# Optimization experiments

Measured on AMD Instinct MI355X. Metric: run time of the kernel, lower is better.

Reference implementation:

```python
import jax, jax.numpy as jnp
import numpy as np

N, E, W, H, NXF, NDF = 131072, 8, 128, 64, 10, 4
DX = 3 + 3 * 2 * NXF  # 63
DV = 3 + 3 * 2 * NDF  # 27
TEMP = 0.166667


def pe(x, degree):
    # positional encoding: [x, sin(2^i x), cos(2^i x)]
    y = jnp.concatenate([(2.0 ** i) * x for i in range(degree)], -1)
    return jnp.concatenate([x, jnp.sin(y), jnp.cos(y)], -1)


def setup_inputs() -> dict:
    key = jax.random.key(0)
    ks = jax.random.split(key, 8)
    s = 0.05
    return {
        'x': jax.random.normal(ks[0], (N, 6), jnp.float32),
        'W_enc': jax.random.normal(ks[1], (DX, W), jnp.float32) * s,
        'b_enc': jnp.zeros((W,), jnp.float32),
        'W_sh': jax.random.normal(ks[2], (E, W, W), jnp.float32) * s,
        'b_sh': jnp.zeros((E, W), jnp.float32),
        'w_sig': jax.random.normal(ks[3], (W,), jnp.float32) * s,
        'b_sig': jnp.zeros((1,), jnp.float32),
        'W_r1': jax.random.normal(ks[4], (E, W + DV, H), jnp.float32) * s,
        'b_r1': jnp.zeros((E, H), jnp.float32),
        'W_r2': jax.random.normal(ks[5], (E, H, 3), jnp.float32) * s,
        'b_r2': jnp.zeros((E, 3), jnp.float32),
    }


def reference(x, W_enc, b_enc, W_sh, b_sh, w_sig, b_sig, W_r1, b_r1, W_r2, b_r2):
    xyz = pe(x[:, :3], NXF)          # [N, 63]
    vd = pe(x[:, 3:6], NDF)          # [N, 27]
    y = jax.nn.relu(xyz @ W_enc + b_enc)  # encoding_xyz -> [N, W]
    # all shape experts at once: [N, E, W]
    shape_out = jax.nn.relu(jnp.einsum('nd,edh->neh', y, W_sh) + b_sh)
    # shared sigma head, softplus keeps sigma > 0: [N, E]
    sigmas = jax.nn.softplus(jnp.einsum('neh,h->ne', shape_out, w_sig) + b_sig)
    log_logits = jax.nn.log_softmax(jnp.log(sigmas + 1e-10) / TEMP, axis=-1)
    # gumbel-softmax (tau=1, torch default) with fixed noise key
    u = jax.random.uniform(jax.random.key(42), sigmas.shape, jnp.float32)
    g = -jnp.log(-jnp.log(u + 1e-20) + 1e-20)
    gates_soft = jax.nn.softmax(log_logits + g, axis=-1)
    index = jnp.argmax(gates_soft, axis=-1)  # [N]
    hard = jax.nn.one_hot(index, E, dtype=sigmas.dtype)
    # straight-through hard gates
    gates_hard = hard - jax.lax.stop_gradient(gates_soft) + gates_soft
    sigmas_pooled = jnp.take_along_axis(sigmas, index[:, None], axis=-1)  # [N, 1]
    # rgb experts: concat(shape_out_i, viewdir) -> MLP -> sigmoid rgb, gated sum
    vdb = jnp.broadcast_to(vd[:, None, :], (vd.shape[0], E, DV))
    inp = jnp.concatenate([shape_out, vdb], axis=-1)  # [N, E, W+27]
    h = jax.nn.relu(jnp.einsum('nec,ech->neh', inp, W_r1) + b_r1)
    rgb = jax.nn.sigmoid(jnp.einsum('neh,eho->neo', h, W_r2) + b_r2)  # [N, E, 3]
    rgbs = jnp.sum(rgb * gates_hard[:, :, None], axis=1)  # [N, 3]
    return jnp.concatenate([rgbs, sigmas_pooled], axis=-1)  # [N, 4]
```

## Files before the change

### kernel.cpp

```cpp
#include <hip/hip_runtime.h>
#include <hip/hip_bf16.h>


#define NPTS 131072
#define PT 64
#define NTH 256
#define NBLK (NPTS / PT)
#define INV2048 (1.0f / 2048.0f)

#define WS_ENC_H 0
#define WS_ENC_L 8192
#define WS_SH_H  16384
#define WS_SH_L  147456
#define WS_R1_H  278528

#define OFF_YH   0
#define OFF_B    17408
#define OFF_RED  38912
#define SMEM_SZ  40960

#define S_LIST(s) (*(int*)(smem + OFF_B + (s) * 336 + 320))
#define S_BID(p)  (*(int*)(smem + OFF_B + (p) * 336 + 324))
#define S_CNT(e)  (*(int*)(smem + OFF_B + (e) * 336 + 328))
#define S_OFF(e)  (*(int*)(smem + OFF_B + (e) * 336 + 332))

typedef __attribute__((ext_vector_type(8))) _Float16 f16x8;
typedef __attribute__((ext_vector_type(4))) _Float16 f16x4;
typedef __attribute__((ext_vector_type(4))) float f32x4;

#define MFMA(a, b, c) __builtin_amdgcn_mfma_f32_16x16x32_f16((a), (b), (c), 0, 0, 0)

__device__ __forceinline__ unsigned rotl32(unsigned x, int d) {
  return (x << d) | (x >> (32 - d));
}

__device__ __forceinline__ float gumbel_for(unsigned flat) {
  const unsigned k0 = 0u, k1 = 42u;
  const unsigned ks2 = k0 ^ k1 ^ 0x1BD11BDAu;
  unsigned x0 = 0u + k0;
  unsigned x1 = flat + k1;
#define TF_RND(r) { x0 += x1; x1 = rotl32(x1, r); x1 ^= x0; }
  TF_RND(13) TF_RND(15) TF_RND(26) TF_RND(6)
  x0 += k1;  x1 += ks2 + 1u;
  TF_RND(17) TF_RND(29) TF_RND(16) TF_RND(24)
  x0 += ks2; x1 += k0 + 2u;
  TF_RND(13) TF_RND(15) TF_RND(26) TF_RND(6)
  x0 += k0;  x1 += k1 + 3u;
  TF_RND(17) TF_RND(29) TF_RND(16) TF_RND(24)
  x0 += k1;  x1 += ks2 + 4u;
  TF_RND(13) TF_RND(15) TF_RND(26) TF_RND(6)
  x0 += ks2; x1 += k0 + 5u;
#undef TF_RND
  unsigned bits = x0 ^ x1;
  float u = __uint_as_float((bits >> 9) | 0x3f800000u) - 1.0f;
  return -logf(-logf(u + 1e-20f) + 1e-20f);
}

__global__ void prep_kernel(const float* __restrict__ W_enc,
                            const float* __restrict__ W_sh,
                            const float* __restrict__ W_r1,
                            _Float16* __restrict__ ws) {
  int tid = blockIdx.x * 256 + threadIdx.x;
  if (tid < 8192) {
    int tile = tid >> 9, r = tid & 511;
    int kk = r >> 4, cc = r & 15;
    int nt = tile >> 1, kt = tile & 1;
    int k = kt * 32 + kk, n = nt * 16 + cc;
    float v = (k < 63) ? W_enc[k * 128 + n] : 0.0f;
    int off = tile * 512 + (kk >> 3) * 128 + cc * 8 + (kk & 7);
    _Float16 h = (_Float16)v;
    ws[WS_ENC_H + off] = h;
    ws[WS_ENC_L + off] = (_Float16)((v - (float)h) * 2048.0f);
  } else if (tid < 139264) {
    int s = tid - 8192;
    int tile = s >> 9, r = s & 511;
    int kk = r >> 4, cc = r & 15;
    int e = tile >> 5, nt = (tile >> 2) & 7, kt = tile & 3;
    int k = kt * 32 + kk, n = nt * 16 + cc;
    float v = W_sh[e * 16384 + k * 128 + n];
    int off = tile * 512 + (kk >> 3) * 128 + cc * 8 + (kk & 7);
    _Float16 h = (_Float16)v;
    ws[WS_SH_H + off] = h;
    ws[WS_SH_L + off] = (_Float16)((v - (float)h) * 2048.0f);
  } else if (tid < 221184) {
    int s = tid - 139264;
    int tile = s >> 9, r = s & 511;
    int kk = r >> 4, cc = r & 15;
    int e = tile / 20, rr = tile % 20;
    int nt = rr / 5, kt = rr % 5;
    int k = kt * 32 + kk, n = nt * 16 + cc;
    float v = (k < 155) ? W_r1[e * 9920 + k * 64 + n] : 0.0f;
    int off = tile * 512 + (kk >> 3) * 128 + cc * 8 + (kk & 7);
    ws[WS_R1_H + off] = (_Float16)v;
  }
}

__global__ __launch_bounds__(NTH, 3)
void nerf_moe_kernel(const float* __restrict__ x,
                     const float* __restrict__ b_enc,
                     const float* __restrict__ b_sh,
                     const float* __restrict__ w_sig, const float* __restrict__ b_sig,
                     const float* __restrict__ b_r1,
                     const float* __restrict__ W_r2,  const float* __restrict__ b_r2,
                     const _Float16* __restrict__ wsw,
                     float* __restrict__ out) {
  __shared__ __align__(16) unsigned char smem[SMEM_SZ];
  _Float16* sYh  = (_Float16*)(smem + OFF_YH);
  float*    sH   = (float*)(smem + OFF_YH);
  _Float16* sYl  = (_Float16*)(smem + OFF_B);
  _Float16* sPEh = (_Float16*)(smem + OFF_B);
  _Float16* sPEl = (_Float16*)(smem + OFF_B + 9216);
  _Float16* sSB  = (_Float16*)(smem + OFF_B);
  float*    sRed = (float*)(smem + OFF_RED);

  const int t  = threadIdx.x;
  const int w  = t >> 6;
  const int L  = t & 63;
  const int q  = L >> 4;
  const int c  = L & 15;
  const int n0 = blockIdx.x * PT;

  sRed[t] = 0.0f;
  sRed[t + 256] = 0.0f;

  for (int idx = t; idx < PT * 64; idx += NTH) {
    int p = idx >> 6, f = idx & 63;
    const float* xr = x + (size_t)(n0 + p) * 6;
    float v;
    if (f < 3)       v = xr[f];
    else if (f < 33) { int g = f - 3;  v = sinf(xr[g % 3] * (float)(1 << (g / 3))); }
    else if (f < 63) { int g = f - 33; v = cosf(xr[g % 3] * (float)(1 << (g / 3))); }
    else             v = 0.0f;
    _Float16 h = (_Float16)v;
    sPEh[p * 72 + f] = h;
    sPEl[p * 72 + f] = (_Float16)((v - (float)h) * 2048.0f);
  }
  __syncthreads();

  {
    f16x8 beh[2][2], bel[2][2];
    #pragma unroll
    for (int ntL = 0; ntL < 2; ++ntL)
      #pragma unroll
      for (int kt = 0; kt < 2; ++kt) {
        int tile = (2 * w + ntL) * 2 + kt;
        beh[ntL][kt] = *(const f16x8*)(wsw + WS_ENC_H + tile * 512 + L * 8);
        bel[ntL][kt] = *(const f16x8*)(wsw + WS_ENC_L + tile * 512 + L * 8);
      }
    f32x4 a1[4][2], a2[4][2];
    #pragma unroll
    for (int mt = 0; mt < 4; ++mt)
      #pragma unroll
      for (int ntL = 0; ntL < 2; ++ntL) { a1[mt][ntL] = (f32x4)0.0f; a2[mt][ntL] = (f32x4)0.0f; }
    #pragma unroll
    for (int half = 0; half < 2; ++half) {
      f16x8 pah[2][2], pal[2][2];
      #pragma unroll
      for (int m = 0; m < 2; ++m)
        #pragma unroll
        for (int kt = 0; kt < 2; ++kt) {
          int off = ((half * 2 + m) * 16 + c) * 72 + kt * 32 + q * 8;
          pah[m][kt] = *(const f16x8*)(sPEh + off);
          pal[m][kt] = *(const f16x8*)(sPEl + off);
        }
      __builtin_amdgcn_s_setprio(1);
      #pragma unroll
      for (int kt = 0; kt < 2; ++kt)
        #pragma unroll
        for (int m = 0; m < 2; ++m)
          #pragma unroll
          for (int ntL = 0; ntL < 2; ++ntL) {
            int mt = half * 2 + m;
            a1[mt][ntL] = MFMA(pah[m][kt], beh[ntL][kt], a1[mt][ntL]);
            a2[mt][ntL] = MFMA(pah[m][kt], bel[ntL][kt], a2[mt][ntL]);
            a2[mt][ntL] = MFMA(pal[m][kt], beh[ntL][kt], a2[mt][ntL]);
          }
      __builtin_amdgcn_s_setprio(0);
      asm volatile("" ::: "memory");
    }
    __syncthreads();
    float bb0 = b_enc[(2 * w) * 16 + c];
    float bb1 = b_enc[(2 * w + 1) * 16 + c];
    #pragma unroll
    for (int mt = 0; mt < 4; ++mt)
      #pragma unroll
      for (int ntL = 0; ntL < 2; ++ntL) {
        float bb = ntL ? bb1 : bb0;
        int col = (2 * w + ntL) * 16 + c;
        #pragma unroll
        for (int r = 0; r < 4; ++r) {
          float v = fmaxf(a1[mt][ntL][r] + a2[mt][ntL][r] * INV2048 + bb, 0.0f);
          int row = mt * 16 + q * 4 + r;
          _Float16 h = (_Float16)v;
          sYh[row * 136 + col] = h;
          sYl[row * 136 + col] = (_Float16)((v - (float)h) * 2048.0f);
        }
      }
  }
  __syncthreads();

  f16x8 Ah[4][3];
  #pragma unroll
  for (int nt = 0; nt < 4; ++nt)
    #pragma unroll
    for (int kt = 0; kt < 3; ++kt)
      Ah[nt][kt] = *(const f16x8*)(sYh + (nt * 16 + c) * 136 + kt * 32 + q * 8);
  const f32x4 wsv0 = *(const f32x4*)(w_sig + (2 * w) * 16 + q * 4);
  const f32x4 wsv1 = *(const f32x4*)(w_sig + (2 * w + 1) * 16 + q * 4);

  float psum[4] = {0.f, 0.f, 0.f, 0.f};

  #pragma unroll 1
  for (int s = 0; s < 16; ++s) {
    int e = s >> 1, i = s & 1;
    int tbase = (e * 8 + 2 * w + i) * 4;
    f16x8 bh[4], bl[4];
    #pragma unroll
    for (int kt = 0; kt < 4; ++kt) {
      bh[kt] = *(const f16x8*)(wsw + WS_SH_H + (tbase + kt) * 512 + L * 8);
      bl[kt] = *(const f16x8*)(wsw + WS_SH_L + (tbase + kt) * 512 + L * 8);
    }
    f32x4 bb = *(const f32x4*)(b_sh + e * 128 + (2 * w + i) * 16 + q * 4);

    f32x4 a1[4], a2[4];
    #pragma unroll
    for (int nt = 0; nt < 4; ++nt) { a1[nt] = (f32x4)0.0f; a2[nt] = (f32x4)0.0f; }
    __builtin_amdgcn_s_setprio(1);
    #pragma unroll
    for (int kt = 0; kt < 4; ++kt)
      #pragma unroll
      for (int nt = 0; nt < 4; ++nt) {
        f16x8 al = *(const f16x8*)(sYl + (nt * 16 + c) * 136 + kt * 32 + q * 8);
        f16x8 ah;
        if (kt < 3) ah = Ah[nt][kt];
        else        ah = *(const f16x8*)(sYh + (nt * 16 + c) * 136 + kt * 32 + q * 8);
        a1[nt] = MFMA(bh[kt], ah, a1[nt]);
        a2[nt] = MFMA(bl[kt], ah, a2[nt]);
        a2[nt] = MFMA(bh[kt], al, a2[nt]);
      }
    __builtin_amdgcn_s_setprio(0);
    f32x4 wv = (s & 1) ? wsv1 : wsv0;
    #pragma unroll
    for (int nt = 0; nt < 4; ++nt)
      #pragma unroll
      for (int r = 0; r < 4; ++r) {
        float sv = fmaxf(fmaf(a2[nt][r], INV2048, a1[nt][r]) + bb[r], 0.0f);
        psum[nt] = fmaf(sv, wv[r], psum[nt]);
      }
    if (s & 1) {
      #pragma unroll
      for (int nt = 0; nt < 4; ++nt) {
        float v = psum[nt];
        v += __shfl_xor(v, 16);
        v += __shfl_xor(v, 32);
        if (q == 0) atomicAdd(sRed + e * 64 + nt * 16 + c, v);
        psum[nt] = 0.f;
      }
    }
  }
  __syncthreads();

  {
    int pt = t >> 2;
    int eb = (t & 3) * 2;
    float best = -1e30f, bsig = 0.0f;
    int bide = 0;
    const float bs = b_sig[0];
    #pragma unroll
    for (int j = 0; j < 2; ++j) {
      int e = eb + j;
      float s = sRed[e * 64 + pt];
      float dotv = s + bs;
      float sig = fmaxf(dotv, 0.0f) + log1pf(expf(-fabsf(dotv)));
      float z = logf(sig + 1e-10f) / 0.166667f;
      float score = z + gumbel_for((unsigned)((n0 + pt) * 8 + e));
      if (score > best) { best = score; bsig = sig; bide = e; }
    }
    #pragma unroll
    for (int m = 1; m <= 2; m <<= 1) {
      float oS  = __shfl_xor(best, m);
      float oSg = __shfl_xor(bsig, m);
      int   oI  = __shfl_xor(bide, m);
      if (oS > best || (oS == best && oI < bide)) { best = oS; bsig = oSg; bide = oI; }
    }
    if ((t & 3) == 0) {
      S_BID(pt) = bide;
      out[(size_t)(n0 + pt) * 4 + 3] = bsig;
    }
  }
  __syncthreads();

  if (t < 64) {
    int bid = S_BID(t);
    unsigned long long below = t ? ((~0ULL) >> (64 - t)) : 0ULL;
    int off = 0;
    #pragma unroll
    for (int e = 0; e < 8; ++e) {
      unsigned long long m = __ballot(bid == e);
      int cnt = __popcll(m);
      if (t == e) { S_CNT(e) = cnt; S_OFF(e) = off; }
      if (bid == e) {
        int rank = __popcll(m & below);
        S_LIST(off + rank) = t;
      }
      off += cnt;
    }
  }
  __syncthreads();

  for (int idx = t; idx < PT * 32; idx += NTH) {
    int s = idx >> 5, cc = idx & 31;
    int pt = S_LIST(s);
    const float* xr = x + (size_t)(n0 + pt) * 6 + 3;
    float v;
    if (cc < 3)       v = xr[cc];
    else if (cc < 15) { int g = cc - 3;  v = sinf(xr[g % 3] * (float)(1 << (g / 3))); }
    else if (cc < 27) { int g = cc - 15; v = cosf(xr[g % 3] * (float)(1 << (g / 3))); }
    else              v = 0.0f;
    sSB[s * 168 + 128 + cc] = (_Float16)v;
  }
  #pragma unroll 1
  for (int ei = 0; ei < 2; ++ei) {
    int e = 2 * w + ei;
    int cnt = S_CNT(e), off = S_OFF(e);
    for (int base = 0; base < cnt; base += 16) {
      int sidx = base + c; if (sidx >= cnt) sidx = cnt - 1;
      int pt = S_LIST(off + sidx);
      f16x8 yb[4];
      #pragma unroll
      for (int kt = 0; kt < 4; ++kt)
        yb[kt] = *(const f16x8*)(sYh + pt * 136 + kt * 32 + q * 8);
      f32x4 acc[8];
      #pragma unroll
      for (int jt = 0; jt < 8; ++jt) acc[jt] = (f32x4)0.0f;
      #pragma unroll
      for (int jh = 0; jh < 2; ++jh) {
        __builtin_amdgcn_s_setprio(1);
        #pragma unroll
        for (int jt2 = 0; jt2 < 4; ++jt2) {
          int jt = jh * 4 + jt2;
          #pragma unroll
          for (int kt = 0; kt < 4; ++kt) {
            f16x8 a = *(const f16x8*)(wsw + WS_SH_H + ((e * 8 + jt) * 4 + kt) * 512 + L * 8);
            acc[jt] = MFMA(a, yb[kt], acc[jt]);
          }
        }
        __builtin_amdgcn_s_setprio(0);
        asm volatile("" ::: "memory");
      }
      bool wr = (base + c) < cnt;
      int slot = off + base + c;
      #pragma unroll
      for (int jt = 0; jt < 8; ++jt) {
        f32x4 bb = *(const f32x4*)(b_sh + e * 128 + jt * 16 + q * 4);
        f16x4 v;
        #pragma unroll
        for (int r = 0; r < 4; ++r)
          v[r] = (_Float16)fmaxf(acc[jt][r] + bb[r], 0.0f);
        if (wr) *(f16x4*)(sSB + slot * 168 + jt * 16 + q * 4) = v;
      }
    }
  }
  __syncthreads();

  #pragma unroll 1
  for (int ei = 0; ei < 2; ++ei) {
    int e = 2 * w + ei;
    int cnt = S_CNT(e), off = S_OFF(e);
    for (int base = 0; base < cnt; base += 16) {
      int sidx = base + c; if (sidx >= cnt) sidx = cnt - 1;
      int slot = off + sidx;
      f16x8 ag[5];
      #pragma unroll
      for (int kt = 0; kt < 5; ++kt)
        ag[kt] = *(const f16x8*)(sSB + slot * 168 + kt * 32 + q * 8);
      f32x4 hacc[4];
      #pragma unroll
      for (int nt = 0; nt < 4; ++nt) hacc[nt] = (f32x4)0.0f;
      #pragma unroll
      for (int nh = 0; nh < 2; ++nh) {
        __builtin_amdgcn_s_setprio(1);
        #pragma unroll
        for (int nt2 = 0; nt2 < 2; ++nt2) {
          int nt = nh * 2 + nt2;
          #pragma unroll
          for (int kt = 0; kt < 5; ++kt) {
            f16x8 bf = *(const f16x8*)(wsw + WS_R1_H + ((e * 4 + nt) * 5 + kt) * 512 + L * 8);
            hacc[nt] = MFMA(ag[kt], bf, hacc[nt]);
          }
        }
        __builtin_amdgcn_s_setprio(0);
        asm volatile("" ::: "memory");
      }
      #pragma unroll
      for (int nt = 0; nt < 4; ++nt) {
        float bb = b_r1[e * 64 + nt * 16 + c];
        #pragma unroll
        for (int r = 0; r < 4; ++r) {
          int m = q * 4 + r;
          if (base + m < cnt)
            sH[(off + base + m) * 68 + nt * 16 + c] = fmaxf(hacc[nt][r] + bb, 0.0f);
        }
      }
    }
  }
  __syncthreads();

  if (t < 192) {
    int s = t / 3, o = t - s * 3;
    int pt = S_LIST(s);
    int e = S_BID(pt);
    float a = b_r2[e * 3 + o];
    const float* w2 = W_r2 + e * 192 + o;
    #pragma unroll
    for (int jj = 0; jj < 64; jj += 4) {
      f32x4 h4 = *(const f32x4*)(sH + s * 68 + jj);
      a = fmaf(h4.x, w2[jj * 3], a);
      a = fmaf(h4.y, w2[jj * 3 + 3], a);
      a = fmaf(h4.z, w2[jj * 3 + 6], a);
      a = fmaf(h4.w, w2[jj * 3 + 9], a);
    }
    out[(size_t)(n0 + pt) * 4 + o] = 1.0f / (1.0f + expf(-a));
  }
}

extern "C" void kernel_launch(void* const* d_in, const int* in_sizes, int n_in,
                              void* d_out, int out_size, void* d_ws, size_t ws_size,
                              hipStream_t stream) {
  (void)in_sizes; (void)n_in; (void)ws_size; (void)out_size;
  const float* x     = (const float*)d_in[0];
  const float* W_enc = (const float*)d_in[1];
  const float* b_enc = (const float*)d_in[2];
  const float* W_sh  = (const float*)d_in[3];
  const float* b_sh  = (const float*)d_in[4];
  const float* w_sig = (const float*)d_in[5];
  const float* b_sig = (const float*)d_in[6];
  const float* W_r1  = (const float*)d_in[7];
  const float* b_r1  = (const float*)d_in[8];
  const float* W_r2  = (const float*)d_in[9];
  const float* b_r2  = (const float*)d_in[10];
  _Float16* ws = (_Float16*)d_ws;
  float* outp = (float*)d_out;
  prep_kernel<<<864, 256, 0, stream>>>(W_enc, W_sh, W_r1, ws);
  nerf_moe_kernel<<<NBLK, NTH, 0, stream>>>(x, b_enc, b_sh, w_sig, b_sig,
                                            b_r1, W_r2, b_r2, ws, outp);
}
```

Before: 256.5 us.

## Partition shape-expert GEMM by point rows per wave instead of output columns

Each wave now owns 16 points and computes all 128 output columns of every shape expert, keeping its A fragments (high and low halves) in registers. This removes the repeated LDS reads of the low-half activations and the shared-memory atomic accumulation, and with it the zero-init of the reduction buffer. The cost is that every wave now loads the full expert weight tiles from global memory/cache, which is four times more weight traffic per block.

```diff
diff --git a/kernel.cpp b/kernel.cpp
--- a/kernel.cpp
+++ b/kernel.cpp
@@ -120,9 +120,6 @@
   const int c  = L & 15;
   const int n0 = blockIdx.x * PT;
 
-  sRed[t] = 0.0f;
-  sRed[t + 256] = 0.0f;
-
   for (int idx = t; idx < PT * 64; idx += NTH) {
     int p = idx >> 6, f = idx & 63;
     const float* xr = x + (size_t)(n0 + p) * 6;
@@ -199,64 +196,48 @@
   }
   __syncthreads();
 
-  f16x8 Ah[4][3];
+  f16x8 Ahw[4], Alw[4];
   #pragma unroll
-  for (int nt = 0; nt < 4; ++nt)
-    #pragma unroll
-    for (int kt = 0; kt < 3; ++kt)
-      Ah[nt][kt] = *(const f16x8*)(sYh + (nt * 16 + c) * 136 + kt * 32 + q * 8);
-  const f32x4 wsv0 = *(const f32x4*)(w_sig + (2 * w) * 16 + q * 4);
-  const f32x4 wsv1 = *(const f32x4*)(w_sig + (2 * w + 1) * 16 + q * 4);
-
-  float psum[4] = {0.f, 0.f, 0.f, 0.f};
+  for (int kt = 0; kt < 4; ++kt) {
+    Ahw[kt] = *(const f16x8*)(sYh + (w * 16 + c) * 136 + kt * 32 + q * 8);
+    Alw[kt] = *(const f16x8*)(sYl + (w * 16 + c) * 136 + kt * 32 + q * 8);
+  }
+  f32x4 wsv[8];
+  #pragma unroll
+  for (int j = 0; j < 8; ++j)
+    wsv[j] = *(const f32x4*)(w_sig + j * 16 + q * 4);
 
   #pragma unroll 1
-  for (int s = 0; s < 16; ++s) {
-    int e = s >> 1, i = s & 1;
-    int tbase = (e * 8 + 2 * w + i) * 4;
-    f16x8 bh[4], bl[4];
-    #pragma unroll
-    for (int kt = 0; kt < 4; ++kt) {
-      bh[kt] = *(const f16x8*)(wsw + WS_SH_H + (tbase + kt) * 512 + L * 8);
-      bl[kt] = *(const f16x8*)(wsw + WS_SH_L + (tbase + kt) * 512 + L * 8);
-    }
-    f32x4 bb = *(const f32x4*)(b_sh + e * 128 + (2 * w + i) * 16 + q * 4);
-
-    f32x4 a1[4], a2[4];
-    #pragma unroll
-    for (int nt = 0; nt < 4; ++nt) { a1[nt] = (f32x4)0.0f; a2[nt] = (f32x4)0.0f; }
-    __builtin_amdgcn_s_setprio(1);
-    #pragma unroll
-    for (int kt = 0; kt < 4; ++kt)
-      #pragma unroll
-      for (int nt = 0; nt < 4; ++nt) {
-        f16x8 al = *(const f16x8*)(sYl + (nt * 16 + c) * 136 + kt * 32 + q * 8);
-        f16x8 ah;
-        if (kt < 3) ah = Ah[nt][kt];
-        else        ah = *(const f16x8*)(sYh + (nt * 16 + c) * 136 + kt * 32 + q * 8);
-        a1[nt] = MFMA(bh[kt], ah, a1[nt]);
-        a2[nt] = MFMA(bl[kt], ah, a2[nt]);
-        a2[nt] = MFMA(bh[kt], al, a2[nt]);
-      }
-    __builtin_amdgcn_s_setprio(0);
-    f32x4 wv = (s & 1) ? wsv1 : wsv0;
-    #pragma unroll
-    for (int nt = 0; nt < 4; ++nt)
+  for (int e = 0; e < 8; ++e) {
+    float psum = 0.f;
+    #pragma unroll
+    for (int j = 0; j < 8; ++j) {
+      int tbase = (e * 8 + j) * 4;
+      f16x8 bh[4], bl[4];
+      #pragma unroll
+      for (int kt = 0; kt < 4; ++kt) {
+        bh[kt] = *(const f16x8*)(wsw + WS_SH_H + (tbase + kt) * 512 + L * 8);
+        bl[kt] = *(const f16x8*)(wsw + WS_SH_L + (tbase + kt) * 512 + L * 8);
+      }
+      f32x4 bb = *(const f32x4*)(b_sh + e * 128 + j * 16 + q * 4);
+      f32x4 a1 = (f32x4)0.0f, a2 = (f32x4)0.0f;
+      __builtin_amdgcn_s_setprio(1);
+      #pragma unroll
+      for (int kt = 0; kt < 4; ++kt) {
+        a1 = MFMA(bh[kt], Ahw[kt], a1);
+        a2 = MFMA(bl[kt], Ahw[kt], a2);
+        a2 = MFMA(bh[kt], Alw[kt], a2);
+      }
+      __builtin_amdgcn_s_setprio(0);
       #pragma unroll
       for (int r = 0; r < 4; ++r) {
-        float sv = fmaxf(fmaf(a2[nt][r], INV2048, a1[nt][r]) + bb[r], 0.0f);
-        psum[nt] = fmaf(sv, wv[r], psum[nt]);
-      }
-    if (s & 1) {
-      #pragma unroll
-      for (int nt = 0; nt < 4; ++nt) {
-        float v = psum[nt];
-        v += __shfl_xor(v, 16);
-        v += __shfl_xor(v, 32);
-        if (q == 0) atomicAdd(sRed + e * 64 + nt * 16 + c, v);
-        psum[nt] = 0.f;
-      }
-    }
+        float sv = fmaxf(fmaf(a2[r], INV2048, a1[r]) + bb[r], 0.0f);
+        psum = fmaf(sv, wsv[j][r], psum);
+      }
+    }
+    psum += __shfl_xor(psum, 16);
+    psum += __shfl_xor(psum, 32);
+    if (q == 0) sRed[e * 64 + w * 16 + c] = psum;
   }
   __syncthreads();
 
```

Result: slower. 294.3 us (+14.7%).
